# Optimization experiments

Measured on AMD Instinct MI355X. Metric: run time of the kernel, lower is better.

The kernel has to match this reference:

```python
import jax, jax.numpy as jnp
import numpy as np

N = 50000; E = 800000; NFEAT = 128; NHID = 64; CONCAT = 2; NCLASS = 40
D = CONCAT * NHID
BN_EPS = 1e-5


def setup_inputs() -> dict:
    key = jax.random.key(0)
    ks = jax.random.split(key, 16)
    rn = lambda k, s, sc=0.05: jax.random.normal(k, s, jnp.float32) * sc
    return {
        "x1a": rn(ks[0], (N, NFEAT), 1.0),
        "x1b": rn(ks[1], (N, NFEAT), 1.0),
        "x2a": rn(ks[2], (N, NFEAT), 1.0),
        "x2b": rn(ks[3], (N, NFEAT), 1.0),
        "edge_index1": jax.random.randint(ks[4], (2, E), 0, N),
        "edge_index2": jax.random.randint(ks[5], (2, E), 0, N),
        "Wi": rn(ks[6], (CONCAT, NFEAT, NHID)),
        "bi": jnp.zeros((CONCAT, NHID), jnp.float32),
        "gi": jnp.ones((CONCAT, NHID), jnp.float32),
        "bei": jnp.zeros((CONCAT, NHID), jnp.float32),
        "Wm": rn(ks[7], (2, D, D)),
        "bm": jnp.zeros((2, D), jnp.float32),
        "gm": jnp.ones((2, D), jnp.float32),
        "bem": jnp.zeros((2, D), jnp.float32),
        "Wf": rn(ks[8], (D, NCLASS)),
        "bf": jnp.zeros((NCLASS,), jnp.float32),
        "fc1w1_W": rn(ks[9], (D,)),
        "fc1w1_b": jnp.zeros((1,), jnp.float32),
        "fc1w2_W": rn(ks[10], (D,)),
        "fc1w2_b": jnp.zeros((1,), jnp.float32),
        "aws_w1_W": rn(ks[11], (2, D)),
        "aws_w1_b": jnp.zeros((2,), jnp.float32),
        "aws_w2_W": rn(ks[12], (2, D)),
        "aws_w2_b": jnp.zeros((2,), jnp.float32),
        "fcw1_W": rn(ks[13], (NCLASS,)),
        "fcw1_b": jnp.zeros((1,), jnp.float32),
        "fcw2_W": rn(ks[14], (NCLASS,)),
        "fcw2_b": jnp.zeros((1,), jnp.float32),
    }


def _gcn_norm(edge_index, n):
    # GCN symmetric normalization with self-loops (cached=True behaviour)
    loop = jnp.arange(n)
    src = jnp.concatenate([edge_index[0], loop])
    dst = jnp.concatenate([edge_index[1], loop])
    deg = jax.ops.segment_sum(jnp.ones_like(dst, jnp.float32), dst, n)
    dinv = jnp.where(deg > 0, deg ** -0.5, 0.0)
    return src, dst, dinv[src] * dinv[dst]


def _gcn(x, W, b, g):
    # GCNConv: dense projection then sparse scatter-based aggregation
    src, dst, norm = g
    h = x @ W
    agg = jax.ops.segment_sum(h[src] * norm[:, None], dst, x.shape[0])
    return agg + b


def _bn(x, gamma, beta):
    m = x.mean(0)
    v = jnp.mean((x - m) ** 2, axis=0)
    return (x - m) * jax.lax.rsqrt(v + BN_EPS) * gamma + beta


def _gate(x1, x2, w1, b1, w2, b2):
    # sigmoid gates L1-normalized; only the last node's row is used (w[-1,:])
    s1 = jax.nn.sigmoid(jnp.dot(x1[-1], w1) + b1)
    s2 = jax.nn.sigmoid(jnp.dot(x2[-1], w2) + b2)
    t = s1 + s2
    return s1 / t, s2 / t


def _forward(x1a, x1b, x2a, x2b, g1, g2, Wi, bi, gi, bei, Wm, bm, gm, bem,
             Wf, bf, fc1w1_W, fc1w1_b, fc1w2_W, fc1w2_b,
             aws_w1_W, aws_w1_b, aws_w2_W, aws_w2_b,
             fcw1_W, fcw1_b, fcw2_W, fcw2_b):
    xs1, xs2 = (x1a, x1b), (x2a, x2b)
    h1 = jnp.concatenate([jax.nn.relu(_bn(_gcn(xs1[i], Wi[i], bi[i], g1), gi[i], bei[i]))
                          for i in range(CONCAT)], axis=-1)
    h2 = jnp.concatenate([jax.nn.relu(_bn(_gcn(xs2[i], Wi[i], bi[i], g2), gi[i], bei[i]))
                          for i in range(CONCAT)], axis=-1)
    w1, w2 = _gate(h1, h2, fc1w1_W, fc1w1_b[0], fc1w2_W, fc1w2_b[0])
    x = w1 * h1 + w2 * h2
    for i in range(Wm.shape[0]):  # middle layers (n_layers - 2)
        a = jax.nn.relu(_bn(_gcn(x, Wm[i], bm[i], g1), gm[i], bem[i]))
        b = jax.nn.relu(_bn(_gcn(x, Wm[i], bm[i], g2), gm[i], bem[i]))
        w1, w2 = _gate(a, b, aws_w1_W[i], aws_w1_b[i], aws_w2_W[i], aws_w2_b[i])
        x = w1 * a + w2 * b
    p1 = _gcn(x, Wf, bf, g1)
    p2 = _gcn(x, Wf, bf, g2)
    w1, w2 = _gate(p1, p2, fcw1_W, fcw1_b[0], fcw2_W, fcw2_b[0])
    return (w1 * p1 + w2 * p2, p1, p2)


def reference(x1a, x1b, x2a, x2b, edge_index1, edge_index2, Wi, bi, gi, bei,
              Wm, bm, gm, bem, Wf, bf, fc1w1_W, fc1w1_b, fc1w2_W, fc1w2_b,
              aws_w1_W, aws_w1_b, aws_w2_W, aws_w2_b,
              fcw1_W, fcw1_b, fcw2_W, fcw2_b):
    g1 = _gcn_norm(edge_index1, N)
    g2 = _gcn_norm(edge_index2, N)
    return _forward(x1a, x1b, x2a, x2b, g1, g2, Wi, bi, gi, bei, Wm, bm, gm, bem,
                    Wf, bf, fc1w1_W, fc1w1_b, fc1w2_W, fc1w2_b,
                    aws_w1_W, aws_w1_b, aws_w2_W, aws_w2_b,
                    fcw1_W, fcw1_b, fcw2_W, fcw2_b)
```

## Files before the change

kernel.cpp:

```cpp
#include <hip/hip_runtime.h>
#include <hip/hip_fp16.h>


#define DFEAT 128

typedef __attribute__((ext_vector_type(8))) short bf16x8;
typedef __attribute__((ext_vector_type(4))) float f32x4;

__device__ __forceinline__ unsigned short f2bf(float f) {
    unsigned u = __float_as_uint(f);
    u += 0x7fffu + ((u >> 16) & 1u);
    return (unsigned short)(u >> 16);
}
__device__ __forceinline__ float bf2f(unsigned short u) {
    return __uint_as_float((unsigned)u << 16);
}
__device__ __forceinline__ float4 bf4tof4(ushort4 u) {
    return make_float4(__uint_as_float((unsigned)u.x << 16),
                       __uint_as_float((unsigned)u.y << 16),
                       __uint_as_float((unsigned)u.z << 16),
                       __uint_as_float((unsigned)u.w << 16));
}
__device__ __forceinline__ unsigned f2h16(float f) {
    return (unsigned)__half_as_ushort(__float2half(f));
}
__device__ __forceinline__ float h16f(unsigned u) {
    return __half2float(__ushort_as_half((unsigned short)u));
}

constexpr int RANGES = 8;
constexpr int SLICES = 128;
constexpr int MAXRSZ = 6400;

__global__ __launch_bounds__(256) void countR_kernel(
    const int* __restrict__ dst1, const int* __restrict__ dst2,
    int* __restrict__ cnt1, int* __restrict__ cnt2, int n, int E, int rsz) {
    int range = blockIdx.x & (RANGES - 1);
    int q = blockIdx.x >> 3;
    int slice = q & (SLICES - 1);
    int graph = q >> 7;
    const int* dst = graph ? dst2 : dst1;
    int* cnt = graph ? cnt2 : cnt1;
    int r0 = range * rsz;
    int rn = min(rsz, n - r0);
    if (rn <= 0) return;
    __shared__ int hist[MAXRSZ];
    int t = threadIdx.x;
    for (int i = t; i < rn; i += 256) hist[i] = 0;
    __syncthreads();
    int es = (E + SLICES - 1) / SLICES;
    int e0 = slice * es;
    int e1 = min(e0 + es, E);
    for (int i = e0 + t; i < e1; i += 256) {
        unsigned d = (unsigned)(dst[i] - r0);
        if (d < (unsigned)rn) atomicAdd(&hist[d], 1);
    }
    __syncthreads();
    for (int i = t; i < rn; i += 256) {
        int v = hist[i];
        if (v) atomicAdd(&cnt[r0 + i], v);
    }
}

__global__ __launch_bounds__(256) void fillR_kernel(
    const int* __restrict__ src1, const int* __restrict__ dst1,
    const int* __restrict__ src2, const int* __restrict__ dst2,
    const int* __restrict__ rp1, const int* __restrict__ rp2,
    const float* __restrict__ dv1, const float* __restrict__ dv2,
    int* __restrict__ fl1, int* __restrict__ fl2,
    int* __restrict__ cs1, int* __restrict__ cs2, int n, int E, int rsz) {
    int range = blockIdx.x & (RANGES - 1);
    int q = blockIdx.x >> 3;
    int slice = q & (SLICES - 1);
    int graph = q >> 7;
    const int *src, *dst, *rp;
    const float* dv;
    int *fl, *cs;
    if (graph == 0) { src = src1; dst = dst1; rp = rp1; dv = dv1; fl = fl1; cs = cs1; }
    else            { src = src2; dst = dst2; rp = rp2; dv = dv2; fl = fl2; cs = cs2; }
    int r0 = range * rsz;
    int rn = min(rsz, n - r0);
    if (rn <= 0) return;
    int es = (E + SLICES - 1) / SLICES;
    int e0 = slice * es;
    int e1 = min(e0 + es, E);
    for (int i = e0 + (int)threadIdx.x; i < e1; i += 256) {
        int d = dst[i];
        if ((unsigned)(d - r0) < (unsigned)rn) {
            int s = src[i];
            float w = dv[d] * dv[s];
            int pos = rp[d] + atomicAdd(&fl[d], 1);
            cs[pos] = (int)((f2h16(w) << 16) | (unsigned)s);
        }
    }
}

__global__ __launch_bounds__(256) void blocksum_kernel(const int* __restrict__ c1,
                                                       const int* __restrict__ c2,
                                                       int* __restrict__ bs, int n, int nb) {
    const int* c = blockIdx.y ? c2 : c1;
    int* out = bs + (size_t)blockIdx.y * nb;
    int t = threadIdx.x;
    int base = blockIdx.x * 2048 + t * 8;
    int s = 0;
#pragma unroll
    for (int i = 0; i < 8; ++i) {
        int idx = base + i;
        if (idx < n) s += c[idx];
    }
    __shared__ int red[256];
    red[t] = s;
    __syncthreads();
    for (int o = 128; o > 0; o >>= 1) {
        if (t < o) red[t] += red[t + o];
        __syncthreads();
    }
    if (t == 0) out[blockIdx.x] = red[0];
}

__global__ void scansums_kernel(int* __restrict__ bs, int nb, int* __restrict__ rp1,
                                int* __restrict__ rp2, int n, int E, float* __restrict__ stats) {
    int t = threadIdx.x;
    if (t < 2) {
        int* b = bs + (size_t)t * nb;
        int run = 0;
        for (int i = 0; i < nb; ++i) {
            int v = b[i];
            b[i] = run;
            run += v;
        }
        (t ? rp2 : rp1)[n] = E;
    }
    for (int i = t; i < 512; i += 64) stats[i] = 0.f;
}

__global__ __launch_bounds__(256) void writerp_kernel(const int* __restrict__ c1,
                                                      const int* __restrict__ c2,
                                                      const int* __restrict__ bs,
                                                      int* __restrict__ rp1, int* __restrict__ rp2,
                                                      float* __restrict__ dv1,
                                                      float* __restrict__ dv2, int n, int nb) {
    const int* c = blockIdx.y ? c2 : c1;
    int* rp = blockIdx.y ? rp2 : rp1;
    float* dv = blockIdx.y ? dv2 : dv1;
    int boff = bs[(size_t)blockIdx.y * nb + blockIdx.x];
    int t = threadIdx.x;
    int base = blockIdx.x * 2048 + t * 8;
    int v[8];
    int s = 0;
#pragma unroll
    for (int i = 0; i < 8; ++i) {
        int idx = base + i;
        v[i] = (idx < n) ? c[idx] : 0;
        s += v[i];
    }
    __shared__ int red[256];
    red[t] = s;
    __syncthreads();
    for (int o = 1; o < 256; o <<= 1) {
        int x = (t >= o) ? red[t - o] : 0;
        __syncthreads();
        red[t] += x;
        __syncthreads();
    }
    int run = boff + red[t] - s;
#pragma unroll
    for (int i = 0; i < 8; ++i) {
        int idx = base + i;
        if (idx < n) {
            rp[idx] = run;
            dv[idx] = rsqrtf((float)(v[i] + 1));
            run += v[i];
        }
    }
}

template <int FV, typename OutT>
__global__ __launch_bounds__(256) void dualagg_kernel(
    const unsigned short* __restrict__ h1, const unsigned short* __restrict__ h2,
    const int* __restrict__ rp1, const int* __restrict__ cs1, const float* __restrict__ dv1,
    const int* __restrict__ rp2, const int* __restrict__ cs2, const float* __restrict__ dv2,
    const float* __restrict__ bias, OutT* __restrict__ o1, OutT* __restrict__ o2, int n) {
    constexpr int COLS = FV * 4;
    const unsigned short* h;
    const int *rp, *cs;
    const float* dv;
    OutT* out;
    if (blockIdx.y == 0) { h = h1; rp = rp1; cs = cs1; dv = dv1; out = o1; }
    else                 { h = h2; rp = rp2; cs = cs2; dv = dv2; out = o2; }
    int wid = blockIdx.x * 4 + (threadIdx.x >> 6);
    if (wid >= n) return;
    int lane = threadIdx.x & 63;
    int half = lane >> 5;
    int l = lane & 31;
    bool act = (l < FV);
    float4 acc = make_float4(0.f, 0.f, 0.f, 0.f);
    int e0 = rp[wid], e1 = rp[wid + 1];
    int e = e0 + half;
    for (; e + 6 < e1; e += 8) {
        int va = cs[e], vb = cs[e + 2], vc = cs[e + 4], vd = cs[e + 6];
        float wa = h16f((unsigned)va >> 16); int sa = va & 0xFFFF;
        float wb = h16f((unsigned)vb >> 16); int sb = vb & 0xFFFF;
        float wc = h16f((unsigned)vc >> 16); int sc = vc & 0xFFFF;
        float wd = h16f((unsigned)vd >> 16); int sd = vd & 0xFFFF;
        if (act) {
            float4 ha = bf4tof4(((const ushort4*)(h + (size_t)sa * COLS))[l]);
            float4 hb = bf4tof4(((const ushort4*)(h + (size_t)sb * COLS))[l]);
            float4 hc = bf4tof4(((const ushort4*)(h + (size_t)sc * COLS))[l]);
            float4 hd = bf4tof4(((const ushort4*)(h + (size_t)sd * COLS))[l]);
            acc.x = fmaf(wa, ha.x, acc.x); acc.y = fmaf(wa, ha.y, acc.y);
            acc.z = fmaf(wa, ha.z, acc.z); acc.w = fmaf(wa, ha.w, acc.w);
            acc.x = fmaf(wb, hb.x, acc.x); acc.y = fmaf(wb, hb.y, acc.y);
            acc.z = fmaf(wb, hb.z, acc.z); acc.w = fmaf(wb, hb.w, acc.w);
            acc.x = fmaf(wc, hc.x, acc.x); acc.y = fmaf(wc, hc.y, acc.y);
            acc.z = fmaf(wc, hc.z, acc.z); acc.w = fmaf(wc, hc.w, acc.w);
            acc.x = fmaf(wd, hd.x, acc.x); acc.y = fmaf(wd, hd.y, acc.y);
            acc.z = fmaf(wd, hd.z, acc.z); acc.w = fmaf(wd, hd.w, acc.w);
        }
    }
    for (; e < e1; e += 2) {
        int va = cs[e];
        float wa = h16f((unsigned)va >> 16); int sa = va & 0xFFFF;
        if (act) {
            float4 ha = bf4tof4(((const ushort4*)(h + (size_t)sa * COLS))[l]);
            acc.x = fmaf(wa, ha.x, acc.x); acc.y = fmaf(wa, ha.y, acc.y);
            acc.z = fmaf(wa, ha.z, acc.z); acc.w = fmaf(wa, ha.w, acc.w);
        }
    }
    acc.x += __shfl_xor(acc.x, 32);
    acc.y += __shfl_xor(acc.y, 32);
    acc.z += __shfl_xor(acc.z, 32);
    acc.w += __shfl_xor(acc.w, 32);
    if (half == 0 && act) {
        float dn = dv[wid];
        float w = dn * dn;
        float4 hv = bf4tof4(((const ushort4*)(h + (size_t)wid * COLS))[l]);
        acc.x = fmaf(w, hv.x, acc.x); acc.y = fmaf(w, hv.y, acc.y);
        acc.z = fmaf(w, hv.z, acc.z); acc.w = fmaf(w, hv.w, acc.w);
        float4 b = ((const float4*)bias)[l];
        acc.x += b.x; acc.y += b.y; acc.z += b.z; acc.w += b.w;
        if constexpr (sizeof(OutT) == 4) {
            ((float4*)((float*)out + (size_t)wid * COLS))[l] = acc;
        } else {
            ushort4 o;
            o.x = f2bf(acc.x); o.y = f2bf(acc.y); o.z = f2bf(acc.z); o.w = f2bf(acc.w);
            ((ushort4*)((unsigned short*)out + (size_t)wid * COLS))[l] = o;
        }
    }
}

__global__ __launch_bounds__(256) void gemm_l1_kernel(
    const float* __restrict__ x1a, const float* __restrict__ x1b, const float* __restrict__ x2a,
    const float* __restrict__ x2b, const float* __restrict__ Wi, unsigned short* __restrict__ H1,
    unsigned short* __restrict__ H2, int nrows) {
    constexpr int CG = 16;
    const float* X = (blockIdx.y == 0) ? x1a : (blockIdx.y == 1) ? x1b
                     : (blockIdx.y == 2) ? x2a : x2b;
    const float* W = Wi + (blockIdx.y & 1) * 128 * 64;
    unsigned short* Y = (blockIdx.y < 2) ? H1 : H2;
    int ocol = (int)(blockIdx.y & 1) * 64;
    __shared__ float Ws[32][64];
    __shared__ float Xs[64][32];
    int tid = threadIdx.x;
    int row0 = blockIdx.x * 64;
    int cg = tid % CG;
    int rg = tid / CG;
    float4 acc[4];
#pragma unroll
    for (int i = 0; i < 4; ++i) acc[i] = make_float4(0.f, 0.f, 0.f, 0.f);
    for (int kc = 0; kc < 4; ++kc) {
        for (int i = tid; i < 32 * CG; i += 256) {
            int r = i / CG, c = i % CG;
            *(float4*)&Ws[r][c * 4] = *(const float4*)(W + (size_t)(kc * 32 + r) * 64 + c * 4);
        }
        for (int i = tid; i < 64 * 8; i += 256) {
            int r = i / 8, c = i % 8;
            int gr = row0 + r;
            float4 v = make_float4(0.f, 0.f, 0.f, 0.f);
            if (gr < nrows) v = *(const float4*)(X + (size_t)gr * DFEAT + kc * 32 + c * 4);
            *(float4*)&Xs[r][c * 4] = v;
        }
        __syncthreads();
#pragma unroll
        for (int k = 0; k < 32; ++k) {
            float4 w = *(float4*)&Ws[k][cg * 4];
#pragma unroll
            for (int i = 0; i < 4; ++i) {
                float a = Xs[rg * 4 + i][k];
                acc[i].x = fmaf(a, w.x, acc[i].x);
                acc[i].y = fmaf(a, w.y, acc[i].y);
                acc[i].z = fmaf(a, w.z, acc[i].z);
                acc[i].w = fmaf(a, w.w, acc[i].w);
            }
        }
        __syncthreads();
    }
#pragma unroll
    for (int i = 0; i < 4; ++i) {
        int r = row0 + rg * 4 + i;
        if (r < nrows) {
            ushort4 o;
            o.x = f2bf(acc[i].x); o.y = f2bf(acc[i].y);
            o.z = f2bf(acc[i].z); o.w = f2bf(acc[i].w);
            *(ushort4*)(Y + (size_t)r * DFEAT + ocol + cg * 4) = o;
        }
    }
}

__global__ __launch_bounds__(256) void prepW_kernel(const float* __restrict__ Wm,
                                                    unsigned short* __restrict__ Wt) {
    int o = blockIdx.x * 256 + threadIdx.x;
    int l = blockIdx.y;
    int kk = o & 31;
    int col = (o >> 5) & 127;
    int kc = o >> 12;
    int k = kc * 32 + kk;
    Wt[(size_t)l * 16384 + o] = f2bf(Wm[(size_t)l * 16384 + (size_t)k * 128 + col]);
}

__global__ __launch_bounds__(256) void gemm_mfma_kernel(
    const unsigned short* __restrict__ Abf, const unsigned short* __restrict__ Bbf,
    const float* __restrict__ ss, const float* __restrict__ wout,
    const unsigned short* __restrict__ Wt, unsigned short* __restrict__ Y, int nrows) {
    __shared__ short Xs[64][128];
    int tid = threadIdx.x;
    int row0 = blockIdx.x * 64;
    int wave = tid >> 6, lane = tid & 63;
    int m = lane & 15, quad = lane >> 4;
    float w1 = wout[0], w2 = wout[1];
    for (int u = tid; u < 1024; u += 256) {
        int r = u >> 4;
        int col0 = (u & 15) * 8;
        int gr = row0 + r;
        if (gr < nrows) {
#pragma unroll
            for (int hh = 0; hh < 2; ++hh) {
                int c = col0 + hh * 4;
                float4 fa = bf4tof4(*(const ushort4*)(Abf + (size_t)gr * 128 + c));
                float4 fb = bf4tof4(*(const ushort4*)(Bbf + (size_t)gr * 128 + c));
                float4 sa = *(const float4*)(ss + c);
                float4 ha = *(const float4*)(ss + 128 + c);
                float4 sb = *(const float4*)(ss + 256 + c);
                float4 hb = *(const float4*)(ss + 384 + c);
                ushort4 o;
                o.x = f2bf(w1 * fmaxf(fmaf(fa.x, sa.x, ha.x), 0.f) +
                           w2 * fmaxf(fmaf(fb.x, sb.x, hb.x), 0.f));
                o.y = f2bf(w1 * fmaxf(fmaf(fa.y, sa.y, ha.y), 0.f) +
                           w2 * fmaxf(fmaf(fb.y, sb.y, hb.y), 0.f));
                o.z = f2bf(w1 * fmaxf(fmaf(fa.z, sa.z, ha.z), 0.f) +
                           w2 * fmaxf(fmaf(fb.z, sb.z, hb.z), 0.f));
                o.w = f2bf(w1 * fmaxf(fmaf(fa.w, sa.w, ha.w), 0.f) +
                           w2 * fmaxf(fmaf(fb.w, sb.w, hb.w), 0.f));
                *(ushort4*)&Xs[r][c] = o;
            }
        } else {
            ushort4 z = {0, 0, 0, 0};
            *(ushort4*)&Xs[r][col0] = z;
            *(ushort4*)&Xs[r][col0 + 4] = z;
        }
    }
    __syncthreads();
    f32x4 acc[8];
#pragma unroll
    for (int i = 0; i < 8; ++i) acc[i] = (f32x4){0.f, 0.f, 0.f, 0.f};
#pragma unroll
    for (int kc = 0; kc < 4; ++kc) {
        bf16x8 a = *(const bf16x8*)&Xs[wave * 16 + m][kc * 32 + quad * 8];
#pragma unroll
        for (int ct = 0; ct < 8; ++ct) {
            const short* bp = (const short*)(Wt + ((size_t)(kc * 128 + ct * 16 + m) * 32) + quad * 8);
            bf16x8 b = *(const bf16x8*)bp;
            acc[ct] = __builtin_amdgcn_mfma_f32_16x16x32_bf16(a, b, acc[ct], 0, 0, 0);
        }
    }
#pragma unroll
    for (int ct = 0; ct < 8; ++ct) {
#pragma unroll
        for (int i = 0; i < 4; ++i) {
            int gr = row0 + wave * 16 + quad * 4 + i;
            if (gr < nrows) Y[(size_t)gr * 128 + ct * 16 + m] = f2bf(acc[ct][i]);
        }
    }
}

template <int CG, int RPT>
__global__ __launch_bounds__(256) void gemm_fused_kernel(
    const unsigned short* __restrict__ Abf, const unsigned short* __restrict__ Bbf,
    const float* __restrict__ ss, const float* __restrict__ wout, const float* __restrict__ W,
    unsigned short* __restrict__ Y, int nrows, int fout, int ostride) {
    __shared__ float Ws[32][CG * 4];
    __shared__ float Xs[64][32];
    int tid = threadIdx.x;
    int row0 = blockIdx.x * 64;
    int cg = tid % CG;
    int rg = tid / CG;
    float w1 = wout[0], w2 = wout[1];
    float4 acc[RPT];
#pragma unroll
    for (int i = 0; i < RPT; ++i) acc[i] = make_float4(0.f, 0.f, 0.f, 0.f);
    for (int kc = 0; kc < 4; ++kc) {
        for (int i = tid; i < 32 * CG; i += 256) {
            int r = i / CG, c = i % CG;
            float4 w;
            if ((c * 4 + 3) < fout) {
                w = *(const float4*)(W + (size_t)(kc * 32 + r) * fout + c * 4);
            } else {
                float t0 = (c * 4 + 0) < fout ? W[(size_t)(kc * 32 + r) * fout + c * 4 + 0] : 0.f;
                float t1 = (c * 4 + 1) < fout ? W[(size_t)(kc * 32 + r) * fout + c * 4 + 1] : 0.f;
                float t2 = (c * 4 + 2) < fout ? W[(size_t)(kc * 32 + r) * fout + c * 4 + 2] : 0.f;
                float t3 = (c * 4 + 3) < fout ? W[(size_t)(kc * 32 + r) * fout + c * 4 + 3] : 0.f;
                w = make_float4(t0, t1, t2, t3);
            }
            *(float4*)&Ws[r][c * 4] = w;
        }
        for (int i = tid; i < 64 * 8; i += 256) {
            int r = i / 8, c = i % 8;
            int gr = row0 + r;
            int col0 = kc * 32 + c * 4;
            float4 v = make_float4(0.f, 0.f, 0.f, 0.f);
            if (gr < nrows) {
                float4 a = bf4tof4(*(const ushort4*)(Abf + (size_t)gr * DFEAT + col0));
                float4 b = bf4tof4(*(const ushort4*)(Bbf + (size_t)gr * DFEAT + col0));
                float4 scA = *(const float4*)(ss + col0);
                float4 shA = *(const float4*)(ss + DFEAT + col0);
                float4 scB = *(const float4*)(ss + 2 * DFEAT + col0);
                float4 shB = *(const float4*)(ss + 3 * DFEAT + col0);
                v.x = w1 * fmaxf(fmaf(a.x, scA.x, shA.x), 0.f) +
                      w2 * fmaxf(fmaf(b.x, scB.x, shB.x), 0.f);
                v.y = w1 * fmaxf(fmaf(a.y, scA.y, shA.y), 0.f) +
                      w2 * fmaxf(fmaf(b.y, scB.y, shB.y), 0.f);
                v.z = w1 * fmaxf(fmaf(a.z, scA.z, shA.z), 0.f) +
                      w2 * fmaxf(fmaf(b.z, scB.z, shB.z), 0.f);
                v.w = w1 * fmaxf(fmaf(a.w, scA.w, shA.w), 0.f) +
                      w2 * fmaxf(fmaf(b.w, scB.w, shB.w), 0.f);
            }
            *(float4*)&Xs[r][c * 4] = v;
        }
        __syncthreads();
#pragma unroll
        for (int k = 0; k < 32; ++k) {
            float4 w = *(float4*)&Ws[k][cg * 4];
#pragma unroll
            for (int i = 0; i < RPT; ++i) {
                float a = Xs[rg * RPT + i][k];
                acc[i].x = fmaf(a, w.x, acc[i].x);
                acc[i].y = fmaf(a, w.y, acc[i].y);
                acc[i].z = fmaf(a, w.z, acc[i].z);
                acc[i].w = fmaf(a, w.w, acc[i].w);
            }
        }
        __syncthreads();
    }
    if (cg * 4 < fout) {
#pragma unroll
        for (int i = 0; i < RPT; ++i) {
            int r = row0 + rg * RPT + i;
            if (r < nrows) {
                ushort4 o;
                o.x = f2bf(acc[i].x); o.y = f2bf(acc[i].y);
                o.z = f2bf(acc[i].z); o.w = f2bf(acc[i].w);
                *(ushort4*)(Y + (size_t)r * ostride + cg * 4) = o;
            }
        }
    }
}

__global__ __launch_bounds__(256) void stats2_kernel(const unsigned short* __restrict__ A,
                                                     const unsigned short* __restrict__ B,
                                                     float* __restrict__ stats, int nrows) {
    __shared__ float red1[256];
    __shared__ float red2[256];
    int t = threadIdx.x;
    int col = t & 127;
    int rg = t >> 7;
    const unsigned short* src = (blockIdx.y == 0) ? A : B;
    float* st = stats + (size_t)blockIdx.y * 256;
    int r0 = blockIdx.x * 128 + rg * 64;
    int r1 = min(r0 + 64, nrows);
    float s = 0.f, s2 = 0.f;
    for (int r = r0; r < r1; ++r) {
        float v = bf2f(src[(size_t)r * DFEAT + col]);
        s += v;
        s2 = fmaf(v, v, s2);
    }
    red1[t] = s;
    red2[t] = s2;
    __syncthreads();
    if (t < 128) {
        atomicAdd(&st[col], red1[t] + red1[t + 128]);
        atomicAdd(&st[DFEAT + col], red2[t] + red2[t + 128]);
    }
}

__global__ __launch_bounds__(128) void gate_prep_kernel(
    float* __restrict__ statsA, float* __restrict__ statsB,
    const unsigned short* __restrict__ preA, const unsigned short* __restrict__ preB,
    const float* __restrict__ gamma, const float* __restrict__ beta,
    const float* __restrict__ gwA, const float* __restrict__ gbA,
    const float* __restrict__ gwB, const float* __restrict__ gbB,
    float* __restrict__ ss, float* __restrict__ wout, int nrows) {
    __shared__ float red[128];
    __shared__ float dotA_s;
    int t = threadIdx.x;
    float invN = 1.f / (float)nrows;
    float meanA = statsA[t] * invN;
    float varA = statsA[DFEAT + t] * invN - meanA * meanA;
    float scA = gamma[t] * rsqrtf(varA + 1e-5f);
    float shA = beta[t] - meanA * scA;
    ss[t] = scA;
    ss[DFEAT + t] = shA;
    float meanB = statsB[t] * invN;
    float varB = statsB[DFEAT + t] * invN - meanB * meanB;
    float scB = gamma[t] * rsqrtf(varB + 1e-5f);
    float shB = beta[t] - meanB * scB;
    ss[2 * DFEAT + t] = scB;
    ss[3 * DFEAT + t] = shB;
    statsA[t] = 0.f;
    statsA[DFEAT + t] = 0.f;
    statsB[t] = 0.f;
    statsB[DFEAT + t] = 0.f;
    float av = fmaxf(fmaf(bf2f(preA[(size_t)(nrows - 1) * DFEAT + t]), scA, shA), 0.f);
    red[t] = av * gwA[t];
    __syncthreads();
    for (int s = 64; s > 0; s >>= 1) {
        if (t < s) red[t] += red[t + s];
        __syncthreads();
    }
    if (t == 0) dotA_s = red[0];
    __syncthreads();
    float bv = fmaxf(fmaf(bf2f(preB[(size_t)(nrows - 1) * DFEAT + t]), scB, shB), 0.f);
    red[t] = bv * gwB[t];
    __syncthreads();
    for (int s = 64; s > 0; s >>= 1) {
        if (t < s) red[t] += red[t + s];
        __syncthreads();
    }
    if (t == 0) {
        float s1 = 1.f / (1.f + expf(-(dotA_s + gbA[0])));
        float s2 = 1.f / (1.f + expf(-(red[0] + gbB[0])));
        float tt = s1 + s2;
        wout[0] = s1 / tt;
        wout[1] = s2 / tt;
    }
}

__global__ __launch_bounds__(64) void gate_final_kernel(
    const float* __restrict__ p1, const float* __restrict__ p2,
    const float* __restrict__ w1v, const float* __restrict__ b1,
    const float* __restrict__ w2v, const float* __restrict__ b2,
    float* __restrict__ wout, int nrows, int nclass) {
    __shared__ float red[64];
    __shared__ float dot1_s;
    int t = threadIdx.x;
    float v = (t < nclass) ? p1[(size_t)(nrows - 1) * nclass + t] * w1v[t] : 0.f;
    red[t] = v;
    __syncthreads();
    for (int s = 32; s > 0; s >>= 1) {
        if (t < s) red[t] += red[t + s];
        __syncthreads();
    }
    if (t == 0) dot1_s = red[0];
    __syncthreads();
    v = (t < nclass) ? p2[(size_t)(nrows - 1) * nclass + t] * w2v[t] : 0.f;
    red[t] = v;
    __syncthreads();
    for (int s = 32; s > 0; s >>= 1) {
        if (t < s) red[t] += red[t + s];
        __syncthreads();
    }
    if (t == 0) {
        float s1 = 1.f / (1.f + expf(-(dot1_s + b1[0])));
        float s2 = 1.f / (1.f + expf(-(red[0] + b2[0])));
        float tt = s1 + s2;
        wout[0] = s1 / tt;
        wout[1] = s2 / tt;
    }
}

__global__ __launch_bounds__(256) void mix_kernel(const float* __restrict__ p1,
                                                  const float* __restrict__ p2,
                                                  const float* __restrict__ wout,
                                                  float* __restrict__ o, int n4) {
    int idx = blockIdx.x * blockDim.x + threadIdx.x;
    if (idx >= n4) return;
    float w1 = wout[0], w2 = wout[1];
    float4 a = *(const float4*)(p1 + (size_t)idx * 4);
    float4 b = *(const float4*)(p2 + (size_t)idx * 4);
    float4 r = make_float4(w1 * a.x + w2 * b.x, w1 * a.y + w2 * b.y, w1 * a.z + w2 * b.z,
                           w1 * a.w + w2 * b.w);
    *(float4*)(o + (size_t)idx * 4) = r;
}

extern "C" void kernel_launch(void* const* d_in, const int* in_sizes, int n_in, void* d_out,
                              int out_size, void* d_ws, size_t ws_size, hipStream_t stream) {
    (void)n_in; (void)out_size; (void)ws_size;
    const int N = in_sizes[0] / DFEAT;
    const int E = in_sizes[4] / 2;
    const int NC = in_sizes[15];

    const float* x1a = (const float*)d_in[0];
    const float* x1b = (const float*)d_in[1];
    const float* x2a = (const float*)d_in[2];
    const float* x2b = (const float*)d_in[3];
    const int* ei1 = (const int*)d_in[4];
    const int* ei2 = (const int*)d_in[5];
    const float* Wi = (const float*)d_in[6];
    const float* bi = (const float*)d_in[7];
    const float* gi = (const float*)d_in[8];
    const float* bei = (const float*)d_in[9];
    const float* Wm = (const float*)d_in[10];
    const float* bm = (const float*)d_in[11];
    const float* gm = (const float*)d_in[12];
    const float* bem = (const float*)d_in[13];
    const float* Wf = (const float*)d_in[14];
    const float* bf = (const float*)d_in[15];
    const float* fc1w1_W = (const float*)d_in[16];
    const float* fc1w1_b = (const float*)d_in[17];
    const float* fc1w2_W = (const float*)d_in[18];
    const float* fc1w2_b = (const float*)d_in[19];
    const float* aws_w1_W = (const float*)d_in[20];
    const float* aws_w1_b = (const float*)d_in[21];
    const float* aws_w2_W = (const float*)d_in[22];
    const float* aws_w2_b = (const float*)d_in[23];
    const float* fcw1_W = (const float*)d_in[24];
    const float* fcw1_b = (const float*)d_in[25];
    const float* fcw2_W = (const float*)d_in[26];
    const float* fcw2_b = (const float*)d_in[27];

    char* ws = (char*)d_ws;
    size_t off = 0;
    auto alloc = [&](size_t bytes) -> char* {
        char* p = ws + off;
        off += (bytes + 255) & ~(size_t)255;
        return p;
    };
    unsigned short* A = (unsigned short*)alloc((size_t)N * DFEAT * 2);
    unsigned short* B = (unsigned short*)alloc((size_t)N * DFEAT * 2);
    unsigned short* H1 = (unsigned short*)alloc((size_t)N * DFEAT * 2);
    unsigned short* H2 = (unsigned short*)alloc((size_t)N * DFEAT * 2);
    int* rp1 = (int*)alloc((size_t)(N + 1) * 4);
    int* rp2 = (int*)alloc((size_t)(N + 1) * 4);
    int* zb = (int*)alloc((size_t)4 * N * 4);
    int* cnt1 = zb;
    int* cnt2 = zb + N;
    int* fl1 = zb + 2 * N;
    int* fl2 = zb + 3 * N;
    float* dv1 = (float*)alloc((size_t)N * 4);
    float* dv2 = (float*)alloc((size_t)N * 4);
    int* cs1 = (int*)alloc((size_t)E * 4);
    int* cs2 = (int*)alloc((size_t)E * 4);
    unsigned short* Wt = (unsigned short*)alloc((size_t)2 * 16384 * 2);
    float* stats = (float*)alloc(2048);
    float* statsA = stats;
    float* statsB = stats + 256;
    float* ssbuf = (float*)alloc(2048);
    float* wout = (float*)alloc(256);
    int nb = (N + 2047) / 2048;
    int* bsums = (int*)alloc((size_t)2 * nb * 4);

    const int* src1 = ei1;
    const int* dst1 = ei1 + E;
    const int* src2 = ei2;
    const int* dst2 = ei2 + E;

    int rsz = (N + RANGES - 1) / RANGES;
    int gemmbl = (N + 63) / 64;
    dim3 rgrid1d(RANGES * SLICES * 2);
    dim3 agggrid((N + 3) / 4, 2);
    dim3 statgrid((N + 127) / 128, 2);
    dim3 scangrid(nb, 2);
    dim3 l1grid(gemmbl, 4);
    dim3 prepgrid(64, 2);

    hipMemsetAsync(zb, 0, (size_t)4 * N * 4, stream);
    prepW_kernel<<<prepgrid, 256, 0, stream>>>(Wm, Wt);
    countR_kernel<<<rgrid1d, 256, 0, stream>>>(dst1, dst2, cnt1, cnt2, N, E, rsz);
    blocksum_kernel<<<scangrid, 256, 0, stream>>>(cnt1, cnt2, bsums, N, nb);
    scansums_kernel<<<1, 64, 0, stream>>>(bsums, nb, rp1, rp2, N, E, stats);
    writerp_kernel<<<scangrid, 256, 0, stream>>>(cnt1, cnt2, bsums, rp1, rp2, dv1, dv2, N, nb);
    fillR_kernel<<<rgrid1d, 256, 0, stream>>>(src1, dst1, src2, dst2, rp1, rp2, dv1, dv2,
                                              fl1, fl2, cs1, cs2, N, E, rsz);

    gemm_l1_kernel<<<l1grid, 256, 0, stream>>>(x1a, x1b, x2a, x2b, Wi, H1, H2, N);
    dualagg_kernel<32, unsigned short><<<agggrid, 256, 0, stream>>>(
        H1, H2, rp1, cs1, dv1, rp2, cs2, dv2, bi, A, B, N);
    stats2_kernel<<<statgrid, 256, 0, stream>>>(A, B, stats, N);
    gate_prep_kernel<<<1, 128, 0, stream>>>(statsA, statsB, A, B, gi, bei, fc1w1_W, fc1w1_b,
                                            fc1w2_W, fc1w2_b, ssbuf, wout, N);

    gemm_mfma_kernel<<<gemmbl, 256, 0, stream>>>(A, B, ssbuf, wout, Wt, H1, N);
    dualagg_kernel<32, unsigned short><<<agggrid, 256, 0, stream>>>(
        H1, H1, rp1, cs1, dv1, rp2, cs2, dv2, bm, A, B, N);
    stats2_kernel<<<statgrid, 256, 0, stream>>>(A, B, stats, N);
    gate_prep_kernel<<<1, 128, 0, stream>>>(statsA, statsB, A, B, gm, bem, aws_w1_W, aws_w1_b,
                                            aws_w2_W, aws_w2_b, ssbuf, wout, N);

    gemm_mfma_kernel<<<gemmbl, 256, 0, stream>>>(A, B, ssbuf, wout, Wt + 16384, H1, N);
    dualagg_kernel<32, unsigned short><<<agggrid, 256, 0, stream>>>(
        H1, H1, rp1, cs1, dv1, rp2, cs2, dv2, bm + 128, A, B, N);
    stats2_kernel<<<statgrid, 256, 0, stream>>>(A, B, stats, N);
    gate_prep_kernel<<<1, 128, 0, stream>>>(statsA, statsB, A, B, gm + 128, bem + 128,
                                            aws_w1_W + 128, aws_w1_b + 1, aws_w2_W + 128,
                                            aws_w2_b + 1, ssbuf, wout, N);

    float* out0 = (float*)d_out;
    float* p1 = out0 + (size_t)N * NC;
    float* p2 = out0 + (size_t)2 * N * NC;
    gemm_fused_kernel<16, 4><<<gemmbl, 256, 0, stream>>>(A, B, ssbuf, wout, Wf, H2, N, NC, NC);
    dualagg_kernel<10, float><<<agggrid, 256, 0, stream>>>(H2, H2, rp1, cs1, dv1, rp2, cs2, dv2,
                                                           bf, p1, p2, N);
    gate_final_kernel<<<1, 64, 0, stream>>>(p1, p2, fcw1_W, fcw1_b, fcw2_W, fcw2_b, wout, N, NC);
    mix_kernel<<<(N * NC / 4 + 255) / 256, 256, 0, stream>>>(p1, p2, wout, out0, N * NC / 4);
}
```

Measured before the change: 763.3 us.

## Build CSR with per-slice histograms and shared-memory fill offsets instead of global atomics

Replaces the global-atomic count and fill of the CSR build with per-(slice,range) histograms written to a buffer, a per-node exclusive scan across slices, and a fill kernel that takes its write positions from shared-memory atomics seeded with the slice offsets. This removes the global atomics on cnt and fl and the memset of four N-sized buffers. In exchange it adds a 2*32*N int buffer that is written and read back, one extra kernel launch, and fewer slices (32 instead of 128), so each block processes more edges. Shared-memory atomics also make the order of entries within a row deterministic per slice.

```diff
diff --git a/kernel.cpp b/kernel.cpp
--- a/kernel.cpp
+++ b/kernel.cpp
@@ -29,18 +29,17 @@
 }
 
 constexpr int RANGES = 8;
-constexpr int SLICES = 128;
+constexpr int SLICES = 32;
 constexpr int MAXRSZ = 6400;
 
-__global__ __launch_bounds__(256) void countR_kernel(
+__global__ __launch_bounds__(256) void histRS_kernel(
     const int* __restrict__ dst1, const int* __restrict__ dst2,
-    int* __restrict__ cnt1, int* __restrict__ cnt2, int n, int E, int rsz) {
+    int* __restrict__ base, int n, int E, int rsz) {
     int range = blockIdx.x & (RANGES - 1);
     int q = blockIdx.x >> 3;
     int slice = q & (SLICES - 1);
-    int graph = q >> 7;
+    int graph = q >> 5;
     const int* dst = graph ? dst2 : dst1;
-    int* cnt = graph ? cnt2 : cnt1;
     int r0 = range * rsz;
     int rn = min(rsz, n - r0);
     if (rn <= 0) return;
@@ -56,40 +55,60 @@
         if (d < (unsigned)rn) atomicAdd(&hist[d], 1);
     }
     __syncthreads();
-    for (int i = t; i < rn; i += 256) {
-        int v = hist[i];
-        if (v) atomicAdd(&cnt[r0 + i], v);
-    }
-}
-
-__global__ __launch_bounds__(256) void fillR_kernel(
+    int* bp = base + (size_t)(graph * SLICES + slice) * n + r0;
+    for (int i = t; i < rn; i += 256) bp[i] = hist[i];
+}
+
+__global__ __launch_bounds__(256) void slicescan_kernel(
+    int* __restrict__ base, int* __restrict__ cnt1, int* __restrict__ cnt2, int n) {
+    int node = blockIdx.x * 256 + threadIdx.x;
+    int g = blockIdx.y;
+    if (node >= n) return;
+    int* p = base + (size_t)g * SLICES * n + node;
+    int run = 0;
+#pragma unroll
+    for (int s = 0; s < SLICES; ++s) {
+        int v = p[(size_t)s * n];
+        p[(size_t)s * n] = run;
+        run += v;
+    }
+    (g ? cnt2 : cnt1)[node] = run;
+}
+
+__global__ __launch_bounds__(256) void fillRS_kernel(
     const int* __restrict__ src1, const int* __restrict__ dst1,
     const int* __restrict__ src2, const int* __restrict__ dst2,
+    const int* __restrict__ base,
     const int* __restrict__ rp1, const int* __restrict__ rp2,
     const float* __restrict__ dv1, const float* __restrict__ dv2,
-    int* __restrict__ fl1, int* __restrict__ fl2,
     int* __restrict__ cs1, int* __restrict__ cs2, int n, int E, int rsz) {
     int range = blockIdx.x & (RANGES - 1);
     int q = blockIdx.x >> 3;
     int slice = q & (SLICES - 1);
-    int graph = q >> 7;
+    int graph = q >> 5;
     const int *src, *dst, *rp;
     const float* dv;
-    int *fl, *cs;
-    if (graph == 0) { src = src1; dst = dst1; rp = rp1; dv = dv1; fl = fl1; cs = cs1; }
-    else            { src = src2; dst = dst2; rp = rp2; dv = dv2; fl = fl2; cs = cs2; }
+    int* cs;
+    if (graph == 0) { src = src1; dst = dst1; rp = rp1; dv = dv1; cs = cs1; }
+    else            { src = src2; dst = dst2; rp = rp2; dv = dv2; cs = cs2; }
     int r0 = range * rsz;
     int rn = min(rsz, n - r0);
     if (rn <= 0) return;
+    __shared__ int off[MAXRSZ];
+    int t = threadIdx.x;
+    const int* bp = base + (size_t)(graph * SLICES + slice) * n + r0;
+    for (int i = t; i < rn; i += 256) off[i] = bp[i] + rp[r0 + i];
+    __syncthreads();
     int es = (E + SLICES - 1) / SLICES;
     int e0 = slice * es;
     int e1 = min(e0 + es, E);
-    for (int i = e0 + (int)threadIdx.x; i < e1; i += 256) {
+    for (int i = e0 + t; i < e1; i += 256) {
         int d = dst[i];
-        if ((unsigned)(d - r0) < (unsigned)rn) {
+        unsigned dr = (unsigned)(d - r0);
+        if (dr < (unsigned)rn) {
             int s = src[i];
             float w = dv[d] * dv[s];
-            int pos = rp[d] + atomicAdd(&fl[d], 1);
+            int pos = atomicAdd(&off[dr], 1);
             cs[pos] = (int)((f2h16(w) << 16) | (unsigned)s);
         }
     }
@@ -640,15 +659,13 @@
     unsigned short* H2 = (unsigned short*)alloc((size_t)N * DFEAT * 2);
     int* rp1 = (int*)alloc((size_t)(N + 1) * 4);
     int* rp2 = (int*)alloc((size_t)(N + 1) * 4);
-    int* zb = (int*)alloc((size_t)4 * N * 4);
-    int* cnt1 = zb;
-    int* cnt2 = zb + N;
-    int* fl1 = zb + 2 * N;
-    int* fl2 = zb + 3 * N;
+    int* cnt1 = (int*)alloc((size_t)N * 4);
+    int* cnt2 = (int*)alloc((size_t)N * 4);
     float* dv1 = (float*)alloc((size_t)N * 4);
     float* dv2 = (float*)alloc((size_t)N * 4);
     int* cs1 = (int*)alloc((size_t)E * 4);
     int* cs2 = (int*)alloc((size_t)E * 4);
+    int* base = (int*)alloc((size_t)2 * SLICES * N * 4);
     unsigned short* Wt = (unsigned short*)alloc((size_t)2 * 16384 * 2);
     float* stats = (float*)alloc(2048);
     float* statsA = stats;
@@ -665,21 +682,22 @@
 
     int rsz = (N + RANGES - 1) / RANGES;
     int gemmbl = (N + 63) / 64;
-    dim3 rgrid1d(RANGES * SLICES * 2);
+    dim3 rsgrid(RANGES * SLICES * 2);
+    dim3 ssgrid((N + 255) / 256, 2);
     dim3 agggrid((N + 3) / 4, 2);
     dim3 statgrid((N + 127) / 128, 2);
     dim3 scangrid(nb, 2);
     dim3 l1grid(gemmbl, 4);
     dim3 prepgrid(64, 2);
 
-    hipMemsetAsync(zb, 0, (size_t)4 * N * 4, stream);
     prepW_kernel<<<prepgrid, 256, 0, stream>>>(Wm, Wt);
-    countR_kernel<<<rgrid1d, 256, 0, stream>>>(dst1, dst2, cnt1, cnt2, N, E, rsz);
+    histRS_kernel<<<rsgrid, 256, 0, stream>>>(dst1, dst2, base, N, E, rsz);
+    slicescan_kernel<<<ssgrid, 256, 0, stream>>>(base, cnt1, cnt2, N);
     blocksum_kernel<<<scangrid, 256, 0, stream>>>(cnt1, cnt2, bsums, N, nb);
     scansums_kernel<<<1, 64, 0, stream>>>(bsums, nb, rp1, rp2, N, E, stats);
     writerp_kernel<<<scangrid, 256, 0, stream>>>(cnt1, cnt2, bsums, rp1, rp2, dv1, dv2, N, nb);
-    fillR_kernel<<<rgrid1d, 256, 0, stream>>>(src1, dst1, src2, dst2, rp1, rp2, dv1, dv2,
-                                              fl1, fl2, cs1, cs2, N, E, rsz);
+    fillRS_kernel<<<rsgrid, 256, 0, stream>>>(src1, dst1, src2, dst2, base, rp1, rp2,
+                                              dv1, dv2, cs1, cs2, N, E, rsz);
 
     gemm_l1_kernel<<<l1grid, 256, 0, stream>>>(x1a, x1b, x2a, x2b, Wi, H1, H2, N);
     dualagg_kernel<32, unsigned short><<<agggrid, 256, 0, stream>>>(
```

Result: no change. 757.6 us (-0.8%).
